# Performance work log

Hardware: AMD Instinct MI355X
Metric: run time of the kernel (lower is better)

The kernel has to match this reference:

```python
import jax, jax.numpy as jnp
import numpy as np

N_NODES = 100000
N_EDGES = 3200000
IN_DIM = 128
HID = 128
K = 20  # n_gaussians


def gcn_conv(x, src, dst, W, b, n_nodes):
    """PyG GCNConv: add self-loops, symmetric normalization, linear transform.
    out = D^{-1/2} (A + I) D^{-1/2} (x @ W) + b, where D is degree of A+I.
    """
    h = x @ W  # [N, out_dim]
    # degree on A + I (self-loop contributes 1 to every node)
    deg = jax.ops.segment_sum(jnp.ones_like(dst, dtype=h.dtype), dst,
                              num_segments=n_nodes) + 1.0
    dis = jax.lax.rsqrt(deg)  # deg >= 1, safe
    norm = dis[src] * dis[dst]  # [E]
    # gather -> scale -> scatter-add (edges), plus self-loop term dis_i^2 * h_i
    agg = jax.ops.segment_sum(h[src] * norm[:, None], dst,
                              num_segments=n_nodes)
    agg = agg + h * (dis * dis)[:, None]
    return agg + b


def setup_inputs() -> dict:
    key = jax.random.key(0)
    ks = jax.random.split(key, 12)
    x = jax.random.normal(ks[0], (N_NODES, IN_DIM), dtype=jnp.float32)
    edge_index = jax.random.randint(ks[1], (2, N_EDGES), 0, N_NODES, dtype=jnp.int32)
    s = 1.0 / np.sqrt(HID)
    W1 = jax.random.uniform(ks[2], (IN_DIM, HID), jnp.float32, -s, s)
    b1 = jnp.zeros((HID,), jnp.float32)
    W2 = jax.random.uniform(ks[3], (HID, HID), jnp.float32, -s, s)
    b2 = jnp.zeros((HID,), jnp.float32)
    pi_W = jax.random.uniform(ks[4], (HID, K), jnp.float32, -s, s)
    pi_b = jnp.zeros((K,), jnp.float32)
    mu_W = jax.random.uniform(ks[5], (HID, K), jnp.float32, -s, s)
    mu_b = jnp.zeros((K,), jnp.float32)
    ls_W = jax.random.uniform(ks[6], (HID, K), jnp.float32, -s, s)
    ls_b = jnp.zeros((K,), jnp.float32)
    return {"x": x, "edge_index": edge_index, "W1": W1, "b1": b1,
            "W2": W2, "b2": b2, "pi_W": pi_W, "pi_b": pi_b,
            "mu_W": mu_W, "mu_b": mu_b, "ls_W": ls_W, "ls_b": ls_b}


def reference(x, edge_index, W1, b1, W2, b2, pi_W, pi_b, mu_W, mu_b, ls_W, ls_b):
    src, dst = edge_index[0], edge_index[1]
    n = x.shape[0]
    h = jax.nn.relu(gcn_conv(x, src, dst, W1, b1, n))
    h = jax.nn.relu(gcn_conv(h, src, dst, W2, b2, n))
    pi = jax.nn.softmax(h @ pi_W + pi_b, axis=1)
    mu = h @ mu_W + mu_b
    log_sigma = h @ ls_W + ls_b
    return (pi, mu, log_sigma)
```

## Files before the change

### kernel.cpp

```cpp
#include <hip/hip_runtime.h>
#include <hip/hip_fp16.h>
#include <cstdint>
#include <cstddef>

#define IN_DIM 128
#define HID    128
#define NG     20
#define T      4096
#define MAXB   400

__global__ void zero_ints(int* __restrict__ a, int n) {
  int i = blockIdx.x * blockDim.x + threadIdx.x;
  if (i < n) a[i] = 0;
}

__global__ __launch_bounds__(256) void binsort1(const int* __restrict__ src,
    const int* __restrict__ dst, int* __restrict__ tmp, int* __restrict__ bofs,
    int* __restrict__ bintot, int NBC, int E) {
  __shared__ int lhist[MAXB];
  __shared__ int lscan[512];
  __shared__ int lcur[MAXB];
  __shared__ int sbuf[T];
  int tid = threadIdx.x;
  int tile0 = blockIdx.x * T;
  int m = E - tile0; if (m > T) m = T;

  for (int i = tid; i < NBC; i += 256) lhist[i] = 0;
  __syncthreads();

  int dreg[16];
#pragma unroll
  for (int j = 0; j < 16; ++j) {
    int idx = j * 256 + tid;
    dreg[j] = -1;
    if (idx < m) {
      int d = dst[tile0 + idx];
      dreg[j] = d;
      atomicAdd(&lhist[d >> 8], 1);
    }
  }
  __syncthreads();

  int v0 = (tid < NBC) ? lhist[tid] : 0;
  int v1 = (256 + tid < NBC) ? lhist[256 + tid] : 0;
  lscan[tid] = v0; lscan[256 + tid] = v1;
  __syncthreads();
  for (int o = 1; o < 512; o <<= 1) {
    int a0 = (tid >= o) ? lscan[tid - o] : 0;
    int a1 = (256 + tid >= o) ? lscan[256 + tid - o] : 0;
    __syncthreads();
    lscan[tid] += a0; lscan[256 + tid] += a1;
    __syncthreads();
  }
  if (tid < NBC)       lcur[tid]       = lscan[tid] - v0;
  if (256 + tid < NBC) lcur[256 + tid] = lscan[256 + tid] - v1;
  __syncthreads();

  int ST = NBC + 1;
  for (int i = tid; i < NBC; i += 256) bofs[(size_t)blockIdx.x * ST + i] = lcur[i];
  if (tid == 0) bofs[(size_t)blockIdx.x * ST + NBC] = m;
  for (int i = tid; i < NBC; i += 256)
    if (lhist[i]) atomicAdd(&bintot[i], lhist[i]);
  __syncthreads();

#pragma unroll
  for (int j = 0; j < 16; ++j) {
    int idx = j * 256 + tid;
    if (idx < m) {
      int d = dreg[j];
      int s = src[tile0 + idx];
      int slot = atomicAdd(&lcur[d >> 8], 1);
      sbuf[slot] = ((d & 255) << 17) | s;
    }
  }
  __syncthreads();

  int nv = m >> 2;
  int4* out4 = (int4*)(tmp + tile0);
  const int4* sb4 = (const int4*)sbuf;
  for (int i = tid; i < nv; i += 256) out4[i] = sb4[i];
  for (int i = (nv << 2) + tid; i < m; i += 256) tmp[tile0 + i] = sbuf[i];
}

__global__ __launch_bounds__(512) void binscan(const int* __restrict__ bintot,
                                               int* __restrict__ binbase, int NBC) {
  __shared__ int s[512];
  int tid = threadIdx.x;
  int v = (tid < NBC) ? bintot[tid] : 0;
  s[tid] = v;
  __syncthreads();
  for (int o = 1; o < 512; o <<= 1) {
    int t = (tid >= o) ? s[tid - o] : 0;
    __syncthreads();
    s[tid] += t;
    __syncthreads();
  }
  if (tid < NBC) binbase[tid] = s[tid] - v;
}

__global__ __launch_bounds__(512) void binsort2(const int* __restrict__ tmp,
    const int* __restrict__ bofs, const int* __restrict__ binbase,
    int* __restrict__ csrc, int* __restrict__ cnt, float* __restrict__ dis,
    int* __restrict__ offs, int NBC, int nblk, int N) {
  __shared__ int lcnt[256];
  __shared__ int lsc[256];
  __shared__ int lcur2[256];
  int b = blockIdx.x;
  int tid = threadIdx.x;
  if (tid < 256) lcnt[tid] = 0;
  __syncthreads();
  int ST = NBC + 1;
  for (int r = tid; r < nblk; r += 512) {
    int s = bofs[(size_t)r * ST + b];
    int e2 = bofs[(size_t)r * ST + b + 1];
    int base = r * T;
    for (int k = s; k < e2; ++k)
      atomicAdd(&lcnt[tmp[base + k] >> 17], 1);
  }
  __syncthreads();
  if (tid < 256) lsc[tid] = lcnt[tid];
  __syncthreads();
  for (int o = 1; o < 256; o <<= 1) {
    int t = 0;
    if (tid < 256 && tid >= o) t = lsc[tid - o];
    __syncthreads();
    if (tid < 256) lsc[tid] += t;
    __syncthreads();
  }
  int gbase = binbase[b];
  if (tid < 256) {
    int excl = lsc[tid] - lcnt[tid];
    lcur2[tid] = gbase + excl;
    int node = (b << 8) + tid;
    if (node < N) {
      cnt[node] = lcnt[tid];
      dis[node] = rsqrtf((float)lcnt[tid] + 1.0f);
      offs[node] = gbase + excl;
    }
  }
  __syncthreads();
  for (int r = tid; r < nblk; r += 512) {
    int s = bofs[(size_t)r * ST + b];
    int e2 = bofs[(size_t)r * ST + b + 1];
    int base = r * T;
    for (int k = s; k < e2; ++k) {
      int rec = tmp[base + k];
      int pos = atomicAdd(&lcur2[rec >> 17], 1);
      csrc[pos] = rec & 0x1FFFF;
    }
  }
}

#define MT 64
#define KC 64
__global__ __launch_bounds__(256) void gemm128_f16out(const float* __restrict__ A,
                                                      const float* __restrict__ B,
                                                      __half* __restrict__ C, int M) {
  __shared__ float sA[MT][KC + 4];
  __shared__ float sB[KC][128];
  int tid = threadIdx.x;
  int m0 = blockIdx.x * MT;
  int tr = tid >> 4;
  int tc = tid & 15;
  float acc[4][8];
#pragma unroll
  for (int i = 0; i < 4; ++i)
#pragma unroll
    for (int j = 0; j < 8; ++j) acc[i][j] = 0.f;

  for (int k0 = 0; k0 < 128; k0 += KC) {
#pragma unroll
    for (int q = 0; q < 4; ++q) {
      int idx = q * 256 + tid;
      int r = idx >> 4;
      int kk = (idx & 15) << 2;
      float4 v = make_float4(0.f, 0.f, 0.f, 0.f);
      if (m0 + r < M) v = *(const float4*)(A + (size_t)(m0 + r) * 128 + k0 + kk);
      *(float4*)(&sA[r][kk]) = v;
    }
#pragma unroll
    for (int q = 0; q < 8; ++q) {
      int idx = q * 256 + tid;
      int kk = idx >> 5;
      int nn = (idx & 31) << 2;
      *(float4*)(&sB[kk][nn]) = *(const float4*)(B + (size_t)(k0 + kk) * 128 + nn);
    }
    __syncthreads();
#pragma unroll 2
    for (int k = 0; k < KC; k += 4) {
      float4 a0 = *(const float4*)(&sA[tr][k]);
      float4 a1 = *(const float4*)(&sA[tr + 16][k]);
      float4 a2 = *(const float4*)(&sA[tr + 32][k]);
      float4 a3 = *(const float4*)(&sA[tr + 48][k]);
#pragma unroll
      for (int u = 0; u < 4; ++u) {
        float4 blo = *(const float4*)(&sB[k + u][tc * 4]);
        float4 bhi = *(const float4*)(&sB[k + u][64 + tc * 4]);
        float av[4] = {((const float*)&a0)[u], ((const float*)&a1)[u],
                       ((const float*)&a2)[u], ((const float*)&a3)[u]};
        float bl[8] = {blo.x, blo.y, blo.z, blo.w, bhi.x, bhi.y, bhi.z, bhi.w};
#pragma unroll
        for (int i = 0; i < 4; ++i)
#pragma unroll
          for (int j = 0; j < 8; ++j) acc[i][j] = fmaf(av[i], bl[j], acc[i][j]);
      }
    }
    __syncthreads();
  }
#pragma unroll
  for (int i = 0; i < 4; ++i) {
    int r = m0 + tr + 16 * i;
    if (r < M) {
      __half2 p0 = __floats2half2_rn(acc[i][0], acc[i][1]);
      __half2 p1 = __floats2half2_rn(acc[i][2], acc[i][3]);
      __half2 p2 = __floats2half2_rn(acc[i][4], acc[i][5]);
      __half2 p3 = __floats2half2_rn(acc[i][6], acc[i][7]);
      __half2* dst0 = (__half2*)(C + (size_t)r * 128 + tc * 4);
      __half2* dst1 = (__half2*)(C + (size_t)r * 128 + 64 + tc * 4);
      dst0[0] = p0; dst0[1] = p1;
      dst1[0] = p2; dst1[1] = p3;
    }
  }
}

__global__ __launch_bounds__(256) void agg_kernel(const __half* __restrict__ h,
    const int* __restrict__ csrc,
    const int* __restrict__ offs, const int* __restrict__ cnt,
    const float* __restrict__ dis, const float* __restrict__ bias,
    float* __restrict__ out, int n) {
  int wave = threadIdx.x >> 6;
  int lane = threadIdx.x & 63;
  int i = blockIdx.x * 4 + wave;
  if (i >= n) return;
  int c = lane * 2;
  int start = offs[i];
  int m = cnt[i];
  float di = dis[i];
  float ax = 0.f, ay = 0.f;

  for (int base = 0; base < m; base += 64) {
    int mc = m - base; if (mc > 64) mc = 64;
    int   sj = 0;
    float wj = 0.f;
    if (lane < mc) {
      sj = csrc[start + base + lane];
      wj = dis[sj] * di;
    }
    int j = 0;
    for (; j + 4 <= mc; j += 4) {
      int   s0 = __shfl(sj, j);
      int   s1 = __shfl(sj, j + 1);
      int   s2 = __shfl(sj, j + 2);
      int   s3 = __shfl(sj, j + 3);
      float w0 = __shfl(wj, j);
      float w1 = __shfl(wj, j + 1);
      float w2 = __shfl(wj, j + 2);
      float w3 = __shfl(wj, j + 3);
      float2 h0 = __half22float2(*(const __half2*)(h + (size_t)s0 * 128 + c));
      float2 h1 = __half22float2(*(const __half2*)(h + (size_t)s1 * 128 + c));
      float2 h2 = __half22float2(*(const __half2*)(h + (size_t)s2 * 128 + c));
      float2 h3 = __half22float2(*(const __half2*)(h + (size_t)s3 * 128 + c));
      ax = fmaf(h0.x, w0, ax); ay = fmaf(h0.y, w0, ay);
      ax = fmaf(h1.x, w1, ax); ay = fmaf(h1.y, w1, ay);
      ax = fmaf(h2.x, w2, ax); ay = fmaf(h2.y, w2, ay);
      ax = fmaf(h3.x, w3, ax); ay = fmaf(h3.y, w3, ay);
    }
    for (; j < mc; ++j) {
      int   s0 = __shfl(sj, j);
      float w0 = __shfl(wj, j);
      float2 h0 = __half22float2(*(const __half2*)(h + (size_t)s0 * 128 + c));
      ax = fmaf(h0.x, w0, ax); ay = fmaf(h0.y, w0, ay);
    }
  }
  float d2 = di * di;
  float2 hs = __half22float2(*(const __half2*)(h + (size_t)i * 128 + c));
  float2 bv = *(const float2*)(bias + c);
  float vx = fmaf(hs.x, d2, ax) + bv.x;
  float vy = fmaf(hs.y, d2, ay) + bv.y;
  *(float2*)(out + (size_t)i * 128 + c) = make_float2(fmaxf(vx, 0.f), fmaxf(vy, 0.f));
}

__global__ void pack_heads_w(const float* __restrict__ piW, const float* __restrict__ muW,
                             const float* __restrict__ lsW, float* __restrict__ W64) {
  int i = blockIdx.x * 256 + threadIdx.x;
  if (i >= 128 * 64) return;
  int k = i >> 6, j = i & 63;
  float v = 0.f;
  if (j < 20)      v = piW[k * 20 + j];
  else if (j < 40) v = muW[k * 20 + (j - 20)];
  else if (j < 60) v = lsW[k * 20 + (j - 40)];
  W64[i] = v;
}

__global__ __launch_bounds__(256) void gemm_heads(const float* __restrict__ A,
                                                  const float* __restrict__ B,
                                                  float* __restrict__ C, int M) {
  __shared__ float sA[64][KC + 4];
  __shared__ float sB[KC][68];
  int tid = threadIdx.x;
  int m0 = blockIdx.x * 64;
  int tr = tid >> 4;
  int tc = tid & 15;
  float acc[4][4];
#pragma unroll
  for (int i = 0; i < 4; ++i)
#pragma unroll
    for (int j = 0; j < 4; ++j) acc[i][j] = 0.f;

  for (int k0 = 0; k0 < 128; k0 += KC) {
#pragma unroll
    for (int q = 0; q < 4; ++q) {
      int idx = q * 256 + tid;
      int r = idx >> 4;
      int kk = (idx & 15) << 2;
      float4 v = make_float4(0.f, 0.f, 0.f, 0.f);
      if (m0 + r < M) v = *(const float4*)(A + (size_t)(m0 + r) * 128 + k0 + kk);
      *(float4*)(&sA[r][kk]) = v;
    }
#pragma unroll
    for (int q = 0; q < 4; ++q) {
      int idx = q * 256 + tid;
      int kk = idx >> 4;
      int nn = (idx & 15) << 2;
      *(float4*)(&sB[kk][nn]) = *(const float4*)(B + (size_t)(k0 + kk) * 64 + nn);
    }
    __syncthreads();
#pragma unroll 4
    for (int k = 0; k < KC; k += 4) {
      float4 a0 = *(const float4*)(&sA[tr][k]);
      float4 a1 = *(const float4*)(&sA[tr + 16][k]);
      float4 a2 = *(const float4*)(&sA[tr + 32][k]);
      float4 a3 = *(const float4*)(&sA[tr + 48][k]);
#pragma unroll
      for (int u = 0; u < 4; ++u) {
        float4 b = *(const float4*)(&sB[k + u][tc * 4]);
        float av[4] = {((const float*)&a0)[u], ((const float*)&a1)[u],
                       ((const float*)&a2)[u], ((const float*)&a3)[u]};
#pragma unroll
        for (int i = 0; i < 4; ++i) {
          acc[i][0] = fmaf(av[i], b.x, acc[i][0]);
          acc[i][1] = fmaf(av[i], b.y, acc[i][1]);
          acc[i][2] = fmaf(av[i], b.z, acc[i][2]);
          acc[i][3] = fmaf(av[i], b.w, acc[i][3]);
        }
      }
    }
    __syncthreads();
  }
#pragma unroll
  for (int i = 0; i < 4; ++i) {
    int r = m0 + tr + 16 * i;
    if (r < M)
      *(float4*)(C + (size_t)r * 64 + tc * 4) =
          make_float4(acc[i][0], acc[i][1], acc[i][2], acc[i][3]);
  }
}

__global__ __launch_bounds__(256) void heads_post(const float* __restrict__ out60,
    const float* __restrict__ pib, const float* __restrict__ mub,
    const float* __restrict__ lsb, float* __restrict__ out, int n) {
  int wave = threadIdx.x >> 6, lane = threadIdx.x & 63;
  int node = blockIdx.x * 4 + wave;
  if (node >= n) return;
  float v = 0.f;
  if (lane < 60) {
    v = out60[(size_t)node * 64 + lane];
    v += (lane < 20) ? pib[lane] : (lane < 40) ? mub[lane - 20] : lsb[lane - 40];
  }
  float pv = (lane < 20) ? v : -__builtin_inff();
  float mx = pv;
  for (int o = 16; o > 0; o >>= 1) mx = fmaxf(mx, __shfl_down(mx, o, 32));
  mx = __shfl(mx, 0, 32);
  float ev = (lane < 20) ? expf(v - mx) : 0.f;
  float sm = ev;
  for (int o = 16; o > 0; o >>= 1) sm += __shfl_down(sm, o, 32);
  sm = __shfl(sm, 0, 32);

  size_t base = (size_t)n * NG;
  if (lane < 20)      out[(size_t)node * NG + lane] = ev / sm;
  else if (lane < 40) out[base + (size_t)node * NG + (lane - 20)] = v;
  else if (lane < 60) out[2 * base + (size_t)node * NG + (lane - 40)] = v;
}

extern "C" void kernel_launch(void* const* d_in, const int* in_sizes, int n_in,
                              void* d_out, int out_size, void* d_ws, size_t ws_size,
                              hipStream_t stream) {
  const float* x   = (const float*)d_in[0];
  const int*   ei  = (const int*)d_in[1];
  const float* W1  = (const float*)d_in[2];
  const float* b1  = (const float*)d_in[3];
  const float* W2  = (const float*)d_in[4];
  const float* b2  = (const float*)d_in[5];
  const float* piW = (const float*)d_in[6];
  const float* pib = (const float*)d_in[7];
  const float* muW = (const float*)d_in[8];
  const float* mub = (const float*)d_in[9];
  const float* lsW = (const float*)d_in[10];
  const float* lsb = (const float*)d_in[11];
  float* out = (float*)d_out;

  const int N = in_sizes[0] / IN_DIM;
  const int E = in_sizes[1] / 2;
  const int* src = ei;
  const int* dst = ei + E;

  const int NBC  = (N + 255) >> 8;
  const int nblk = (E + T - 1) / T;
  const int ST   = NBC + 1;

  char* p = (char*)d_ws;
  char* regionH = p;                        p += (size_t)N * HID * sizeof(__half);
  __half* h16  = (__half*)regionH;
  float* out60 = (float*)regionH;
  char* regionR = p;
  size_t szR = (size_t)N * HID * sizeof(float);
  size_t szT = (size_t)E * sizeof(int);
  p += (szR > szT ? szR : szT);
  int*   tmp    = (int*)regionR;
  float* bufB   = (float*)regionR;
  int*   csrc   = (int*)p;                  p += (size_t)E * sizeof(int);
  int*   bofs   = (int*)p;                  p += (size_t)nblk * ST * sizeof(int);
  int*   bintot = (int*)p;                  p += (size_t)MAXB * sizeof(int);
  int*   binbase= (int*)p;                  p += (size_t)MAXB * sizeof(int);
  int*   cnt    = (int*)p;                  p += (size_t)N * sizeof(int);
  int*   offs   = (int*)p;                  p += (size_t)N * sizeof(int);
  float* dis    = (float*)p;                p += (size_t)N * sizeof(float);
  float* W64    = (float*)p;                p += (size_t)128 * 64 * sizeof(float);

  zero_ints<<<(NBC + 255) / 256, 256, 0, stream>>>(bintot, NBC);
  binsort1<<<nblk, 256, 0, stream>>>(src, dst, tmp, bofs, bintot, NBC, E);
  binscan<<<1, 512, 0, stream>>>(bintot, binbase, NBC);
  binsort2<<<NBC, 512, 0, stream>>>(tmp, bofs, binbase, csrc, cnt, dis, offs,
                                    NBC, nblk, N);
  pack_heads_w<<<(128 * 64 + 255) / 256, 256, 0, stream>>>(piW, muW, lsW, W64);

  gemm128_f16out<<<(N + MT - 1) / MT, 256, 0, stream>>>(x, W1, h16, N);
  agg_kernel<<<(N + 3) / 4, 256, 0, stream>>>(h16, csrc, offs, cnt, dis, b1, bufB, N);
  gemm128_f16out<<<(N + MT - 1) / MT, 256, 0, stream>>>(bufB, W2, h16, N);
  agg_kernel<<<(N + 3) / 4, 256, 0, stream>>>(h16, csrc, offs, cnt, dis, b2, bufB, N);

  gemm_heads<<<(N + 63) / 64, 256, 0, stream>>>(bufB, W64, out60, N);
  heads_post<<<(N + 3) / 4, 256, 0, stream>>>(out60, pib, mub, lsb, out, N);
}
```

Baseline: 594.1 us.

## Split hidden features into two 64-column halves and aggregate each separately

The GEMM now writes its fp16 output as two separate N×64 arrays instead of one N×128 array. Aggregation runs as two passes, one per half, so each pass gathers from a feature table half the size, which should give the edge gathers better cache locality. Within a pass, each wave splits into two 32-lane groups that process alternating edges, and the partial sums are combined with a cross-half shuffle. The cost is reading the CSR indices and degree weights twice and launching twice as many aggregation kernels.

```diff
diff --git a/kernel.cpp b/kernel.cpp
--- a/kernel.cpp
+++ b/kernel.cpp
@@ -155,7 +155,8 @@
 #define KC 64
 __global__ __launch_bounds__(256) void gemm128_f16out(const float* __restrict__ A,
                                                       const float* __restrict__ B,
-                                                      __half* __restrict__ C, int M) {
+                                                      __half* __restrict__ CA,
+                                                      __half* __restrict__ CB, int M) {
   __shared__ float sA[MT][KC + 4];
   __shared__ float sB[KC][128];
   int tid = threadIdx.x;
@@ -215,24 +216,26 @@
       __half2 p1 = __floats2half2_rn(acc[i][2], acc[i][3]);
       __half2 p2 = __floats2half2_rn(acc[i][4], acc[i][5]);
       __half2 p3 = __floats2half2_rn(acc[i][6], acc[i][7]);
-      __half2* dst0 = (__half2*)(C + (size_t)r * 128 + tc * 4);
-      __half2* dst1 = (__half2*)(C + (size_t)r * 128 + 64 + tc * 4);
-      dst0[0] = p0; dst0[1] = p1;
-      dst1[0] = p2; dst1[1] = p3;
-    }
-  }
-}
-
-__global__ __launch_bounds__(256) void agg_kernel(const __half* __restrict__ h,
+      __half2* dA = (__half2*)(CA + (size_t)r * 64 + tc * 4);
+      __half2* dB = (__half2*)(CB + (size_t)r * 64 + tc * 4);
+      dA[0] = p0; dA[1] = p1;
+      dB[0] = p2; dB[1] = p3;
+    }
+  }
+}
+
+__global__ __launch_bounds__(256) void agg_half(const __half* __restrict__ hh,
     const int* __restrict__ csrc,
     const int* __restrict__ offs, const int* __restrict__ cnt,
     const float* __restrict__ dis, const float* __restrict__ bias,
-    float* __restrict__ out, int n) {
+    float* __restrict__ out, int hx, int n) {
   int wave = threadIdx.x >> 6;
   int lane = threadIdx.x & 63;
   int i = blockIdx.x * 4 + wave;
   if (i >= n) return;
-  int c = lane * 2;
+  int low = lane & 31;
+  int grp = lane >> 5;
+  int c = low * 2;
   int start = offs[i];
   int m = cnt[i];
   float di = dis[i];
@@ -247,37 +250,41 @@
       wj = dis[sj] * di;
     }
     int j = 0;
-    for (; j + 4 <= mc; j += 4) {
-      int   s0 = __shfl(sj, j);
-      int   s1 = __shfl(sj, j + 1);
-      int   s2 = __shfl(sj, j + 2);
-      int   s3 = __shfl(sj, j + 3);
-      float w0 = __shfl(wj, j);
-      float w1 = __shfl(wj, j + 1);
-      float w2 = __shfl(wj, j + 2);
-      float w3 = __shfl(wj, j + 3);
-      float2 h0 = __half22float2(*(const __half2*)(h + (size_t)s0 * 128 + c));
-      float2 h1 = __half22float2(*(const __half2*)(h + (size_t)s1 * 128 + c));
-      float2 h2 = __half22float2(*(const __half2*)(h + (size_t)s2 * 128 + c));
-      float2 h3 = __half22float2(*(const __half2*)(h + (size_t)s3 * 128 + c));
+    for (; j + 8 <= mc; j += 8) {
+      int e0 = j + grp, e1 = j + 2 + grp, e2 = j + 4 + grp, e3 = j + 6 + grp;
+      int   s0 = __shfl(sj, e0), s1 = __shfl(sj, e1);
+      int   s2 = __shfl(sj, e2), s3 = __shfl(sj, e3);
+      float w0 = __shfl(wj, e0), w1 = __shfl(wj, e1);
+      float w2 = __shfl(wj, e2), w3 = __shfl(wj, e3);
+      float2 h0 = __half22float2(*(const __half2*)(hh + (size_t)s0 * 64 + c));
+      float2 h1 = __half22float2(*(const __half2*)(hh + (size_t)s1 * 64 + c));
+      float2 h2 = __half22float2(*(const __half2*)(hh + (size_t)s2 * 64 + c));
+      float2 h3 = __half22float2(*(const __half2*)(hh + (size_t)s3 * 64 + c));
       ax = fmaf(h0.x, w0, ax); ay = fmaf(h0.y, w0, ay);
       ax = fmaf(h1.x, w1, ax); ay = fmaf(h1.y, w1, ay);
       ax = fmaf(h2.x, w2, ax); ay = fmaf(h2.y, w2, ay);
       ax = fmaf(h3.x, w3, ax); ay = fmaf(h3.y, w3, ay);
     }
-    for (; j < mc; ++j) {
-      int   s0 = __shfl(sj, j);
-      float w0 = __shfl(wj, j);
-      float2 h0 = __half22float2(*(const __half2*)(h + (size_t)s0 * 128 + c));
+    for (; j < mc; j += 2) {
+      int e0 = j + grp;
+      int   s0 = __shfl(sj, e0);
+      float w0 = __shfl(wj, e0);
+      float2 h0 = __half22float2(*(const __half2*)(hh + (size_t)s0 * 64 + c));
       ax = fmaf(h0.x, w0, ax); ay = fmaf(h0.y, w0, ay);
     }
   }
-  float d2 = di * di;
-  float2 hs = __half22float2(*(const __half2*)(h + (size_t)i * 128 + c));
-  float2 bv = *(const float2*)(bias + c);
-  float vx = fmaf(hs.x, d2, ax) + bv.x;
-  float vy = fmaf(hs.y, d2, ay) + bv.y;
-  *(float2*)(out + (size_t)i * 128 + c) = make_float2(fmaxf(vx, 0.f), fmaxf(vy, 0.f));
+  ax += __shfl_xor(ax, 32);
+  ay += __shfl_xor(ay, 32);
+
+  if (lane < 32) {
+    float d2 = di * di;
+    float2 hs = __half22float2(*(const __half2*)(hh + (size_t)i * 64 + c));
+    float2 bv = *(const float2*)(bias + c);
+    float vx = fmaf(hs.x, d2, ax) + bv.x;
+    float vy = fmaf(hs.y, d2, ay) + bv.y;
+    *(float2*)(out + (size_t)i * 128 + hx * 64 + c) =
+        make_float2(fmaxf(vx, 0.f), fmaxf(vy, 0.f));
+  }
 }
 
 __global__ void pack_heads_w(const float* __restrict__ piW, const float* __restrict__ muW,
@@ -410,7 +417,8 @@
 
   char* p = (char*)d_ws;
   char* regionH = p;                        p += (size_t)N * HID * sizeof(__half);
-  __half* h16  = (__half*)regionH;
+  __half* hA   = (__half*)regionH;
+  __half* hB   = hA + (size_t)N * 64;
   float* out60 = (float*)regionH;
   char* regionR = p;
   size_t szR = (size_t)N * HID * sizeof(float);
@@ -434,10 +442,12 @@
                                     NBC, nblk, N);
   pack_heads_w<<<(128 * 64 + 255) / 256, 256, 0, stream>>>(piW, muW, lsW, W64);
 
-  gemm128_f16out<<<(N + MT - 1) / MT, 256, 0, stream>>>(x, W1, h16, N);
-  agg_kernel<<<(N + 3) / 4, 256, 0, stream>>>(h16, csrc, offs, cnt, dis, b1, bufB, N);
-  gemm128_f16out<<<(N + MT - 1) / MT, 256, 0, stream>>>(bufB, W2, h16, N);
-  agg_kernel<<<(N + 3) / 4, 256, 0, stream>>>(h16, csrc, offs, cnt, dis, b2, bufB, N);
+  gemm128_f16out<<<(N + MT - 1) / MT, 256, 0, stream>>>(x, W1, hA, hB, N);
+  agg_half<<<(N + 3) / 4, 256, 0, stream>>>(hA, csrc, offs, cnt, dis, b1,      bufB, 0, N);
+  agg_half<<<(N + 3) / 4, 256, 0, stream>>>(hB, csrc, offs, cnt, dis, b1 + 64, bufB, 1, N);
+  gemm128_f16out<<<(N + MT - 1) / MT, 256, 0, stream>>>(bufB, W2, hA, hB, N);
+  agg_half<<<(N + 3) / 4, 256, 0, stream>>>(hA, csrc, offs, cnt, dis, b2,      bufB, 0, N);
+  agg_half<<<(N + 3) / 4, 256, 0, stream>>>(hB, csrc, offs, cnt, dis, b2 + 64, bufB, 1, N);
 
   gemm_heads<<<(N + 63) / 64, 256, 0, stream>>>(bufB, W64, out60, N);
   heads_post<<<(N + 3) / 4, 256, 0, stream>>>(out60, pib, mub, lsb, out, N);
```

Measured after the change: 644.4 us. 1.08x slower.
